# Kernel optimization log

Hardware: AMD Instinct MI355X
Metric: run time of the kernel (lower is better)

Reference implementation:

```python
import jax, jax.numpy as jnp
import numpy as np

HID = 256      # cfg.MODEL.YOSO.HIDDEN_DIM
NPROP = 100    # cfg.MODEL.YOSO.NUM_PROPOSALS
K1 = 3         # CONV_KERNEL_SIZE_1D
K2 = 1         # CONV_KERNEL_SIZE_2D
NCLS = 80      # NUM_CLASSES
NHEAD = 8

def layernorm(x, g, b, eps=1e-5):
    m = jnp.mean(x, -1, keepdims=True)
    v = jnp.var(x, -1, keepdims=True)
    return (x - m) * jax.lax.rsqrt(v + eps) * g + b

def dysep(query, value, Wl, bl, ng, nb):
    # dynamic depthwise conv (kernel K1 along feature axis, one kernel per proposal)
    # followed by dynamic pointwise NxN conv, per torch F.conv1d semantics (cross-correlation, 'same' pad)
    w = query @ Wl + bl                      # [B,N,N+K1]
    dw = w[..., :K1]                         # [B,N,K1] depthwise kernels
    pw = w[..., K1:]                         # [B,N,N]  pointwise mixing
    C = value.shape[-1]
    pad = K1 // 2
    vp = jnp.pad(value, ((0, 0), (0, 0), (pad, pad)))
    depth = sum(dw[..., k:k + 1] * vp[..., k:k + C] for k in range(K1))
    depth = jax.nn.relu(depth)
    point = jnp.einsum('bmn,bnc->bmc', pw, depth)
    return layernorm(point, ng, nb)

def mha(x, in_w, in_b, out_w, out_b):
    B, N, E = x.shape
    d = E // NHEAD
    qkv = x @ in_w + in_b
    q, k, v = jnp.split(qkv, 3, axis=-1)
    q = q.reshape(B, N, NHEAD, d)
    k = k.reshape(B, N, NHEAD, d)
    v = v.reshape(B, N, NHEAD, d)
    att = jnp.einsum('bqhd,bkhd->bhqk', q, k) / jnp.sqrt(jnp.asarray(d, x.dtype))
    att = jax.nn.softmax(att, axis=-1)
    o = jnp.einsum('bhqk,bkhd->bqhd', att, v).reshape(B, N, E)
    return o @ out_w + out_b

def setup_inputs() -> dict:
    key = jax.random.key(0)
    ks = iter(jax.random.split(key, 64))
    B, H, W = 8, 128, 128
    E = HID * K2 * K2
    nrm = lambda *s: jax.random.normal(next(ks), s, jnp.float32) * 0.02
    bias_value = -np.log((1 - 0.01) / 0.01)
    return dict(
        features=jax.random.normal(next(ks), (B, HID, H, W), jnp.float32),
        proposal_kernels=jax.random.normal(next(ks), (B, NPROP, E), jnp.float32),
        mask_preds=jax.random.normal(next(ks), (B, NPROP, H, W), jnp.float32),
        fW=nrm(E, NPROP + K1), fb=jnp.zeros(NPROP + K1), fng=jnp.ones(E), fnb=jnp.zeros(E),
        f_norm_g=jnp.ones(E), f_norm_b=jnp.zeros(E),
        kW=nrm(E, NPROP + K1), kb=jnp.zeros(NPROP + K1), kng=jnp.ones(E), knb=jnp.zeros(E),
        k_norm_g=jnp.ones(E), k_norm_b=jnp.zeros(E),
        attn_in_w=nrm(E, 3 * E), attn_in_b=jnp.zeros(3 * E),
        attn_out_w=nrm(E, E), attn_out_b=jnp.zeros(E),
        s_norm_g=jnp.ones(E), s_norm_b=jnp.zeros(E),
        ffn_w1=nrm(HID, 2048), ffn_b1=jnp.zeros(2048),
        ffn_w2=nrm(2048, HID), ffn_b2=jnp.zeros(HID),
        ffn_norm_g=jnp.ones(HID), ffn_norm_b=jnp.zeros(HID),
        cls_w=nrm(HID, HID), cls_ln_g=jnp.ones(HID), cls_ln_b=jnp.zeros(HID),
        fc_cls_w=nrm(HID, NCLS + 1), fc_cls_b=jnp.full((NCLS + 1,), bias_value, jnp.float32),
        mask_w=nrm(3, HID, HID), mask_ln_g=jnp.ones((3, HID)), mask_ln_b=jnp.zeros((3, HID)),
        fc_mask_w=nrm(HID, HID), fc_mask_b=jnp.zeros(HID),
        train_flag=1,
    )

def reference(features, proposal_kernels, mask_preds, fW, fb, fng, fnb, f_norm_g, f_norm_b,
              kW, kb, kng, knb, k_norm_g, k_norm_b,
              attn_in_w, attn_in_b, attn_out_w, attn_out_b, s_norm_g, s_norm_b,
              ffn_w1, ffn_b1, ffn_w2, ffn_b2, ffn_norm_g, ffn_norm_b,
              cls_w, cls_ln_g, cls_ln_b, fc_cls_w, fc_cls_b,
              mask_w, mask_ln_g, mask_ln_b, fc_mask_w, fc_mask_b, train_flag):
    B, C, H, W = features.shape
    hard = (jax.nn.sigmoid(mask_preds) > 0.5).astype(features.dtype)   # hard masks (no grad path)
    f = jnp.einsum('bnhw,bchw->bnc', hard, features)                   # mask-pooled features [B,N,E]
    k = proposal_kernels.reshape(B, NPROP, -1)
    f = layernorm(f + dysep(k, f, fW, fb, fng, fnb), f_norm_g, f_norm_b)
    kk = layernorm(f + dysep(k, f, kW, kb, kng, knb), k_norm_g, k_norm_b)
    kk = layernorm(kk + mha(kk, attn_in_w, attn_in_b, attn_out_w, attn_out_b), s_norm_g, s_norm_b)
    obj = jnp.transpose(kk.reshape(B, NPROP, HID, -1), (0, 1, 3, 2))   # [B,N,K2*K2,HID]
    h = jax.nn.relu(obj @ ffn_w1 + ffn_b1)
    obj = layernorm(obj + (h @ ffn_w2 + ffn_b2), ffn_norm_g, ffn_norm_b)
    cls_feat = obj.sum(-2)                                             # [B,N,HID]
    mask_feat = obj
    if train_flag:
        cls_feat = jax.nn.relu(layernorm(cls_feat @ cls_w, cls_ln_g, cls_ln_b))
        cls_score = (cls_feat @ fc_cls_w + fc_cls_b).reshape(B, NPROP, -1)
    else:
        cls_score = None
    for i in range(mask_w.shape[0]):
        mask_feat = jax.nn.relu(layernorm(mask_feat @ mask_w[i], mask_ln_g[i], mask_ln_b[i]))
    mask_kernels = (mask_feat @ fc_mask_w + fc_mask_b)[:, :, 0, :]     # squeeze(2), K2*K2==1
    new_mask_preds = jnp.einsum('bqc,bchw->bqhw', mask_kernels, features)
    obj_out = jnp.transpose(obj, (0, 1, 3, 2)).reshape(B, NPROP, HID, K2, K2)
    return (cls_score, new_mask_preds, obj_out)
```

## Files before the change

kernel.cpp:

```cpp
#include <hip/hip_runtime.h>

typedef float f32x4 __attribute__((ext_vector_type(4)));
typedef short bfrag __attribute__((ext_vector_type(8)));
typedef short sh4 __attribute__((ext_vector_type(4)));

__device__ __forceinline__ unsigned short f2bf(float x) {
  unsigned int u = __float_as_uint(x);
  return (unsigned short)((u + 0x7FFFu + ((u >> 16) & 1u)) >> 16);
}
__device__ __forceinline__ float bf2f(unsigned short u) {
  return __uint_as_float(((unsigned int)u) << 16);
}
__device__ __forceinline__ float wred_sum(float v) {
#pragma unroll
  for (int o = 32; o > 0; o >>= 1) v += __shfl_xor(v, o);
  return v;
}
__device__ __forceinline__ float wred_max(float v) {
#pragma unroll
  for (int o = 32; o > 0; o >>= 1) v = fmaxf(v, __shfl_xor(v, o));
  return v;
}

struct Prep12 {
  const float* s[12];
  int K[12];
  int N[12];
  int base[12];
  int doff[12];
};

__global__ __launch_bounds__(256) void prep_w(Prep12 p, unsigned short* wt) {
  int t = blockIdx.x;
  int wi = 0;
#pragma unroll
  for (int i = 0; i < 11; ++i)
    if (t >= p.base[i + 1]) wi = i + 1;
  int lt = t - p.base[wi];
  int K = p.K[wi], N = p.N[wi];
  int tkn = (K + 31) >> 5;
  int tk = lt % tkn, tn = lt / tkn;
  __shared__ float tile[32][33];
  const float* src = p.s[wi];
#pragma unroll
  for (int i = 0; i < 4; ++i) {
    int flat = i * 256 + threadIdx.x;
    int kl = flat >> 5, nl = flat & 31;
    int k = tk * 32 + kl, n = tn * 32 + nl;
    tile[kl][nl] = (k < K && n < N) ? src[(size_t)k * N + n] : 0.f;
  }
  __syncthreads();
  unsigned short* dst = wt + p.doff[wi];
#pragma unroll
  for (int i = 0; i < 4; ++i) {
    int flat = i * 256 + threadIdx.x;
    int nl = flat >> 5, kl = flat & 31;
    int k = tk * 32 + kl, n = tn * 32 + nl;
    if (k < K && n < N) {
      int np = (wi < 2) ? ((n >= 3) ? n - 3 : n + 100) : n;
      dst[(size_t)np * K + k] = f2bf(tile[kl][nl]);
    }
  }
}

__global__ __launch_bounds__(256) void prep_bias(const float* __restrict__ fb_,
                                                 const float* __restrict__ kb_,
                                                 float* __restrict__ bf,
                                                 float* __restrict__ bk) {
  int t = threadIdx.x;
  if (t < 103) {
    int np = (t >= 3) ? t - 3 : t + 100;
    bf[np] = fb_[t];
    bk[np] = kb_[t];
  }
  if (t == 103) { bf[103] = 0.f; bk[103] = 0.f; }
}

template <int ABF, int OBF>
__global__ __launch_bounds__(256) void gemm_mf(const void* Av,
                                               const unsigned short* __restrict__ Wt,
                                               const float* __restrict__ bias,
                                               void* Cv, int M, int K, int N, int ldc, int relu) {
  __shared__ short Al[64 * 72];
  __shared__ short Wl[64 * 72];
  int tid = threadIdx.x;
  int r0 = blockIdx.x * 64;
  int c0 = blockIdx.y * 64;
  int w = tid >> 6, lane = tid & 63, quad = lane >> 4, l15 = lane & 15;

  f32x4 acc[4];
#pragma unroll
  for (int mt = 0; mt < 4; ++mt) {
    acc[mt][0] = 0.f; acc[mt][1] = 0.f; acc[mt][2] = 0.f; acc[mt][3] = 0.f;
  }

  for (int k0 = 0; k0 < K; k0 += 64) {
    if (ABF) {
      const unsigned short* A = (const unsigned short*)Av;
#pragma unroll
      for (int p = 0; p < 2; ++p) {
        int flat = p * 256 + tid;
        int row = flat >> 3, k8 = flat & 7;
        bfrag v;
        if (r0 + row < M)
          v = *(const bfrag*)(A + (size_t)(r0 + row) * K + k0 + k8 * 8);
        else
          v = (bfrag)(short)0;
        *(bfrag*)(Al + row * 72 + k8 * 8) = v;
      }
    } else {
      const float* A = (const float*)Av;
#pragma unroll
      for (int p = 0; p < 4; ++p) {
        int flat = p * 256 + tid;
        int row = flat >> 4, c4 = flat & 15;
        sh4 o4;
        if (r0 + row < M) {
          float4 v = *(const float4*)(A + (size_t)(r0 + row) * K + k0 + c4 * 4);
          o4[0] = (short)f2bf(v.x); o4[1] = (short)f2bf(v.y);
          o4[2] = (short)f2bf(v.z); o4[3] = (short)f2bf(v.w);
        } else {
          o4[0] = 0; o4[1] = 0; o4[2] = 0; o4[3] = 0;
        }
        *(sh4*)(Al + row * 72 + c4 * 4) = o4;
      }
    }
#pragma unroll
    for (int p = 0; p < 2; ++p) {
      int flat = p * 256 + tid;
      int row = flat >> 3, k8 = flat & 7;
      bfrag v;
      if (c0 + row < N)
        v = *(const bfrag*)(Wt + (size_t)(c0 + row) * K + k0 + k8 * 8);
      else
        v = (bfrag)(short)0;
      *(bfrag*)(Wl + row * 72 + k8 * 8) = v;
    }
    __syncthreads();
#pragma unroll
    for (int kk = 0; kk < 2; ++kk) {
      bfrag bv = *(const bfrag*)(Wl + (w * 16 + l15) * 72 + kk * 32 + quad * 8);
#pragma unroll
      for (int mt = 0; mt < 4; ++mt) {
        bfrag av = *(const bfrag*)(Al + (mt * 16 + l15) * 72 + kk * 32 + quad * 8);
        acc[mt] = __builtin_amdgcn_mfma_f32_16x16x32_bf16(av, bv, acc[mt], 0, 0, 0);
      }
    }
    __syncthreads();
  }
  int col = c0 + w * 16 + l15;
  if (col < N) {
    float bv = bias ? bias[col] : 0.f;
#pragma unroll
    for (int mt = 0; mt < 4; ++mt)
#pragma unroll
      for (int r = 0; r < 4; ++r) {
        int m = r0 + mt * 16 + quad * 4 + r;
        if (m < M) {
          float v = acc[mt][r] + bv;
          if (relu) v = fmaxf(v, 0.f);
          if (OBF)
            ((unsigned short*)Cv)[(size_t)m * ldc + col] = f2bf(v);
          else
            ((float*)Cv)[(size_t)m * ldc + col] = v;
        }
      }
  }
}

__global__ __launch_bounds__(512, 4) void phaseA(const float* __restrict__ mask,
                                                 const float* __restrict__ feat,
                                                 float* __restrict__ partial) {
  int tid = threadIdx.x;
  int ks = blockIdx.x;
  int ct = blockIdx.y;
  int b  = blockIdx.z;
  __shared__ short Al[112 * 136];
  __shared__ short Bl[128 * 136];
  int w = tid >> 6, lane = tid & 63, quad = lane >> 4, l15 = lane & 15;

  f32x4 acc[7];
#pragma unroll
  for (int mt = 0; mt < 7; ++mt) {
    acc[mt][0] = 0.f; acc[mt][1] = 0.f; acc[mt][2] = 0.f; acc[mt][3] = 0.f;
  }

  int k0 = ks * 512;
  for (int st = 0; st < 4; ++st) {
    int kb = k0 + st * 128;
#pragma unroll
    for (int p = 0; p < 7; ++p) {
      int flat = p * 512 + tid;
      int row = flat >> 5, c4 = flat & 31;
      sh4 o4;
      if (row < 100) {
        float4 v = *(const float4*)(mask + (size_t)(b * 100 + row) * 16384 + kb + c4 * 4);
        o4[0] = (v.x > 0.f) ? (short)0x3F80 : (short)0;
        o4[1] = (v.y > 0.f) ? (short)0x3F80 : (short)0;
        o4[2] = (v.z > 0.f) ? (short)0x3F80 : (short)0;
        o4[3] = (v.w > 0.f) ? (short)0x3F80 : (short)0;
      } else {
        o4[0] = 0; o4[1] = 0; o4[2] = 0; o4[3] = 0;
      }
      *(sh4*)(Al + row * 136 + c4 * 4) = o4;
    }
#pragma unroll
    for (int p = 0; p < 8; ++p) {
      int flat = p * 512 + tid;
      int row = flat >> 5, c4 = flat & 31;
      float4 v = *(const float4*)(feat + (size_t)(b * 256 + ct * 128 + row) * 16384 + kb + c4 * 4);
      sh4 o4;
      o4[0] = (short)f2bf(v.x); o4[1] = (short)f2bf(v.y);
      o4[2] = (short)f2bf(v.z); o4[3] = (short)f2bf(v.w);
      *(sh4*)(Bl + row * 136 + c4 * 4) = o4;
    }
    __syncthreads();
#pragma unroll
    for (int kk = 0; kk < 4; ++kk) {
      bfrag bv = *(const bfrag*)(Bl + (w * 16 + l15) * 136 + kk * 32 + quad * 8);
#pragma unroll
      for (int mt = 0; mt < 7; ++mt) {
        bfrag av = *(const bfrag*)(Al + (mt * 16 + l15) * 136 + kk * 32 + quad * 8);
        acc[mt] = __builtin_amdgcn_mfma_f32_16x16x32_bf16(av, bv, acc[mt], 0, 0, 0);
      }
    }
    __syncthreads();
  }
  float* pb = partial + (size_t)(b * 32 + ks) * (100 * 256) + ct * 128 + w * 16 + l15;
#pragma unroll
  for (int mt = 0; mt < 7; ++mt)
#pragma unroll
    for (int r = 0; r < 4; ++r) {
      int m = mt * 16 + quad * 4 + r;
      if (m < 100) pb[(size_t)m * 256] = acc[mt][r];
    }
}

__global__ __launch_bounds__(256) void reduceA(const float* __restrict__ partial,
                                               float* __restrict__ fm) {
  int gid = blockIdx.x * 256 + threadIdx.x;
  int c = gid & 255, row = gid >> 8;
  int b = row / 100, n = row % 100;
  float s = 0.f;
#pragma unroll
  for (int ks = 0; ks < 32; ++ks)
    s += partial[((size_t)(b * 32 + ks) * 100 + n) * 256 + c];
  fm[(size_t)row * 256 + c] = s;
}

__global__ __launch_bounds__(256) void pointdw(const float* __restrict__ fm,
                                               const float* __restrict__ wbuf,
                                               float* __restrict__ point) {
  int tid = threadIdx.x;
  int b = blockIdx.y, c0 = blockIdx.x * 32;
  __shared__ float dl[100 * 33];
  for (int flat = tid; flat < 3200; flat += 256) {
    int n = flat >> 5, cl = flat & 31, c = c0 + cl;
    const float* fr = fm + (size_t)(b * 100 + n) * 256;
    const float* wr = wbuf + (size_t)(b * 100 + n) * 104;
    float x0 = (c > 0) ? fr[c - 1] : 0.f;
    float x1 = fr[c];
    float x2 = (c < 255) ? fr[c + 1] : 0.f;
    float d = wr[100] * x0 + wr[101] * x1 + wr[102] * x2;
    dl[n * 33 + cl] = fmaxf(d, 0.f);
  }
  __syncthreads();
  int cl = tid & 31, mg = tid >> 5;
  for (int m = mg; m < 100; m += 8) {
    const float4* pw4 = (const float4*)(wbuf + (size_t)(b * 100 + m) * 104);
    float a = 0.f;
#pragma unroll
    for (int n4 = 0; n4 < 25; ++n4) {
      float4 wv = pw4[n4];
      a += wv.x * dl[(n4 * 4 + 0) * 33 + cl] + wv.y * dl[(n4 * 4 + 1) * 33 + cl]
         + wv.z * dl[(n4 * 4 + 2) * 33 + cl] + wv.w * dl[(n4 * 4 + 3) * 33 + cl];
    }
    point[(size_t)(b * 100 + m) * 256 + c0 + cl] = a;
  }
}

__global__ __launch_bounds__(256) void ln2_kernel(const float* __restrict__ x,
                                                  const float* __restrict__ resid,
                                                  const float* __restrict__ g1, const float* __restrict__ b1,
                                                  const float* __restrict__ g2, const float* __restrict__ b2,
                                                  float* __restrict__ out) {
  int tid = threadIdx.x;
  int row = blockIdx.x * 4 + (tid >> 6);
  int lane = tid & 63;
  size_t base = (size_t)row * 256 + lane * 4;
  float4 v = *(const float4*)(x + base);
  float mean = wred_sum(v.x + v.y + v.z + v.w) * (1.f / 256.f);
  float d0 = v.x - mean, d1 = v.y - mean, d2 = v.z - mean, d3 = v.w - mean;
  float rs = rsqrtf(wred_sum(d0 * d0 + d1 * d1 + d2 * d2 + d3 * d3) * (1.f / 256.f) + 1e-5f);
  float4 gv = *(const float4*)(g1 + lane * 4);
  float4 bv = *(const float4*)(b1 + lane * 4);
  float4 rv = *(const float4*)(resid + base);
  float y0 = rv.x + d0 * rs * gv.x + bv.x;
  float y1 = rv.y + d1 * rs * gv.y + bv.y;
  float y2 = rv.z + d2 * rs * gv.z + bv.z;
  float y3 = rv.w + d3 * rs * gv.w + bv.w;
  float mean2 = wred_sum(y0 + y1 + y2 + y3) * (1.f / 256.f);
  float e0 = y0 - mean2, e1 = y1 - mean2, e2 = y2 - mean2, e3 = y3 - mean2;
  float rs2 = rsqrtf(wred_sum(e0 * e0 + e1 * e1 + e2 * e2 + e3 * e3) * (1.f / 256.f) + 1e-5f);
  float4 g2v = *(const float4*)(g2 + lane * 4);
  float4 b2v = *(const float4*)(b2 + lane * 4);
  float4 o;
  o.x = e0 * rs2 * g2v.x + b2v.x;
  o.y = e1 * rs2 * g2v.y + b2v.y;
  o.z = e2 * rs2 * g2v.z + b2v.z;
  o.w = e3 * rs2 * g2v.w + b2v.w;
  *(float4*)(out + base) = o;
}

__global__ __launch_bounds__(256) void ln_kernel(const float* __restrict__ x,
                                                 const float* __restrict__ res,
                                                 const float* __restrict__ g, const float* __restrict__ bb,
                                                 float* __restrict__ out, int relu,
                                                 float* __restrict__ copy2) {
  int tid = threadIdx.x;
  int row = blockIdx.x * 4 + (tid >> 6);
  int lane = tid & 63;
  size_t base = (size_t)row * 256 + lane * 4;
  float4 v = *(const float4*)(x + base);
  if (res) {
    float4 rv = *(const float4*)(res + base);
    v.x += rv.x; v.y += rv.y; v.z += rv.z; v.w += rv.w;
  }
  float mean = wred_sum(v.x + v.y + v.z + v.w) * (1.f / 256.f);
  float d0 = v.x - mean, d1 = v.y - mean, d2 = v.z - mean, d3 = v.w - mean;
  float rs = rsqrtf(wred_sum(d0 * d0 + d1 * d1 + d2 * d2 + d3 * d3) * (1.f / 256.f) + 1e-5f);
  float4 gv = *(const float4*)(g + lane * 4);
  float4 bv = *(const float4*)(bb + lane * 4);
  float4 o;
  o.x = d0 * rs * gv.x + bv.x;
  o.y = d1 * rs * gv.y + bv.y;
  o.z = d2 * rs * gv.z + bv.z;
  o.w = d3 * rs * gv.w + bv.w;
  if (relu) {
    o.x = fmaxf(o.x, 0.f); o.y = fmaxf(o.y, 0.f);
    o.z = fmaxf(o.z, 0.f); o.w = fmaxf(o.w, 0.f);
  }
  *(float4*)(out + base) = o;
  if (copy2) *(float4*)(copy2 + base) = o;
}

__global__ __launch_bounds__(256) void attn_kernel(const float* __restrict__ qkv,
                                                   float* __restrict__ obuf) {
  int tid = threadIdx.x;
  int b = blockIdx.y, h = blockIdx.x;
  __shared__ float ktj[100 * 32];
  __shared__ unsigned short vl[100 * 32];
  __shared__ float sl[100 * 100];
  const float* base = qkv + (size_t)b * 100 * 768;
  for (int flat = tid; flat < 3200; flat += 256) {
    int j = flat >> 5, dd = flat & 31;
    ktj[j * 32 + dd] = base[(size_t)j * 768 + 256 + h * 32 + dd];
    vl[j * 32 + dd] = f2bf(base[(size_t)j * 768 + 512 + h * 32 + dd]);
  }
  __syncthreads();
  {
    int i = tid >> 1;
    int jh = (tid & 1) * 50;
    int qi = (i < 100) ? i : 0;
    const float4* q4 = (const float4*)(base + (size_t)qi * 768 + h * 32);
    float4 q[8];
#pragma unroll
    for (int d4 = 0; d4 < 8; ++d4) q[d4] = q4[d4];
    if (i < 100) {
      for (int jj = 0; jj < 50; ++jj) {
        int j = jh + jj;
        const float4* kr = (const float4*)(ktj + j * 32);
        float a = 0.f;
#pragma unroll
        for (int d4 = 0; d4 < 8; ++d4) {
          float4 kv = kr[d4];
          a += q[d4].x * kv.x + q[d4].y * kv.y + q[d4].z * kv.z + q[d4].w * kv.w;
        }
        sl[i * 100 + j] = a * 0.17677669529663687f;
      }
    }
  }
  __syncthreads();
  int w = tid >> 6, lane = tid & 63;
  for (int r = w; r < 100; r += 4) {
    float x0 = sl[r * 100 + lane];
    float x1 = (lane + 64 < 100) ? sl[r * 100 + lane + 64] : -1e30f;
    float mx = wred_max(fmaxf(x0, x1));
    float e0 = __expf(x0 - mx);
    float e1 = (lane + 64 < 100) ? __expf(x1 - mx) : 0.f;
    float inv = 1.f / wred_sum(e0 + e1);
    sl[r * 100 + lane] = e0 * inv;
    if (lane + 64 < 100) sl[r * 100 + lane + 64] = e1 * inv;
  }
  __syncthreads();
  for (int flat = tid; flat < 3200; flat += 256) {
    int i = flat >> 5, dd = flat & 31;
    float a = 0.f;
#pragma unroll 4
    for (int j = 0; j < 100; ++j) a += sl[i * 100 + j] * bf2f(vl[j * 32 + dd]);
    obuf[(size_t)(b * 100 + i) * 256 + h * 32 + dd] = a;
  }
}

__global__ __launch_bounds__(256) void phaseE(const float* __restrict__ mk,
                                              const float* __restrict__ feat,
                                              float* __restrict__ out) {
  int tid = threadIdx.x;
  int b = blockIdx.y;
  int hw0 = blockIdx.x * 128;
  __shared__ short Al[112 * 264];
#pragma unroll
  for (int p = 0; p < 28; ++p) {
    int flat = p * 256 + tid;
    int row = flat >> 6, c4 = flat & 63;
    sh4 o4;
    if (row < 100) {
      float4 v = *(const float4*)(mk + (size_t)(b * 100 + row) * 256 + c4 * 4);
      o4[0] = (short)f2bf(v.x); o4[1] = (short)f2bf(v.y);
      o4[2] = (short)f2bf(v.z); o4[3] = (short)f2bf(v.w);
    } else {
      o4[0] = 0; o4[1] = 0; o4[2] = 0; o4[3] = 0;
    }
    *(sh4*)(Al + row * 264 + c4 * 4) = o4;
  }
  __syncthreads();
  int w = tid >> 6, lane = tid & 63, quad = lane >> 4, l15 = lane & 15;
  f32x4 acc[7][2];
#pragma unroll
  for (int mt = 0; mt < 7; ++mt)
#pragma unroll
    for (int nt = 0; nt < 2; ++nt) {
      acc[mt][nt][0] = 0.f; acc[mt][nt][1] = 0.f; acc[mt][nt][2] = 0.f; acc[mt][nt][3] = 0.f;
    }
  size_t fb = (size_t)b * 256 * 16384;
  int hwl = hw0 + w * 32 + l15;
  for (int kk = 0; kk < 8; ++kk) {
    bfrag bv[2];
#pragma unroll
    for (int nt = 0; nt < 2; ++nt) {
#pragma unroll
      for (int j = 0; j < 8; ++j) {
        float v = feat[fb + (size_t)(kk * 32 + quad * 8 + j) * 16384 + hwl + nt * 16];
        bv[nt][j] = (short)f2bf(v);
      }
    }
    bfrag av[7];
#pragma unroll
    for (int mt = 0; mt < 7; ++mt)
      av[mt] = *(const bfrag*)(Al + (mt * 16 + l15) * 264 + kk * 32 + quad * 8);
#pragma unroll
    for (int mt = 0; mt < 7; ++mt) {
      acc[mt][0] = __builtin_amdgcn_mfma_f32_16x16x32_bf16(av[mt], bv[0], acc[mt][0], 0, 0, 0);
      acc[mt][1] = __builtin_amdgcn_mfma_f32_16x16x32_bf16(av[mt], bv[1], acc[mt][1], 0, 0, 0);
    }
  }
#pragma unroll
  for (int mt = 0; mt < 7; ++mt)
#pragma unroll
    for (int nt = 0; nt < 2; ++nt)
#pragma unroll
      for (int r = 0; r < 4; ++r) {
        int m = mt * 16 + quad * 4 + r;
        if (m < 100)
          out[(size_t)(b * 100 + m) * 16384 + hw0 + w * 32 + nt * 16 + l15] = acc[mt][nt][r];
      }
}

extern "C" void kernel_launch(void* const* d_in, const int* in_sizes, int n_in,
                              void* d_out, int out_size, void* d_ws, size_t ws_size,
                              hipStream_t stream) {
  const float* feat    = (const float*)d_in[0];
  const float* prop    = (const float*)d_in[1];
  const float* maskp   = (const float*)d_in[2];
  const float* fW      = (const float*)d_in[3];
  const float* fb_     = (const float*)d_in[4];
  const float* fng     = (const float*)d_in[5];
  const float* fnb     = (const float*)d_in[6];
  const float* f_ng    = (const float*)d_in[7];
  const float* f_nb    = (const float*)d_in[8];
  const float* kW      = (const float*)d_in[9];
  const float* kb_     = (const float*)d_in[10];
  const float* kng     = (const float*)d_in[11];
  const float* knb     = (const float*)d_in[12];
  const float* k_ng    = (const float*)d_in[13];
  const float* k_nb    = (const float*)d_in[14];
  const float* aw_in   = (const float*)d_in[15];
  const float* ab_in   = (const float*)d_in[16];
  const float* aw_out  = (const float*)d_in[17];
  const float* ab_out  = (const float*)d_in[18];
  const float* s_ng    = (const float*)d_in[19];
  const float* s_nb    = (const float*)d_in[20];
  const float* w1      = (const float*)d_in[21];
  const float* b1      = (const float*)d_in[22];
  const float* w2      = (const float*)d_in[23];
  const float* b2      = (const float*)d_in[24];
  const float* ffn_ng  = (const float*)d_in[25];
  const float* ffn_nb  = (const float*)d_in[26];
  const float* cls_w   = (const float*)d_in[27];
  const float* cls_g   = (const float*)d_in[28];
  const float* cls_b   = (const float*)d_in[29];
  const float* fcclsw  = (const float*)d_in[30];
  const float* fcclsb  = (const float*)d_in[31];
  const float* mask_w  = (const float*)d_in[32];
  const float* mask_g  = (const float*)d_in[33];
  const float* mask_b  = (const float*)d_in[34];
  const float* fcmw    = (const float*)d_in[35];
  const float* fcmb    = (const float*)d_in[36];
  float* out = (float*)d_out;

  float* ws = (float*)d_ws;
  size_t off = 0;
  unsigned short* wt = (unsigned short*)(ws + off); off += 856192;
  float* fm     = ws + off; off += 204800;
  float* bias_f = ws + off; off += 104;
  float* bias_k = ws + off; off += 104;
  float* partial = ws + off;
  float* ub = partial;
  size_t uo = 0;
  float* wb   = ub + uo; uo += 83200;
  float* pt   = ub + uo; uo += 204800;
  float* fbuf = ub + uo; uo += 204800;
  float* kkb  = ub + uo; uo += 204800;
  float* qkvb = ub + uo; uo += 614400;
  float* ob   = ub + uo; uo += 204800;
  float* mo   = ub + uo; uo += 204800;
  float* kk2  = ub + uo; uo += 204800;
  float* t1   = ub + uo; uo += 204800;
  float* objb = ub + uo; uo += 204800;
  float* t2   = ub + uo; uo += 204800;
  float* mkb  = ub + uo; uo += 204800;
  unsigned short* ffn1b = (unsigned short*)(ub + uo); uo += 409600;

  const int wt_fW = 0, wt_kW = 26624, wt_ain = 53248, wt_aout = 249856;
  const int wt_w1 = 315392, wt_w2 = 839680, wt_cls = 1363968, wt_fccls = 1429504;
  const int wt_m0 = 1450240, wt_m1 = 1515776, wt_m2 = 1581312, wt_fcm = 1646848;

  float* out_cls  = out;
  float* out_mask = out + 64800;
  float* out_obj  = out + 64800 + 13107200;

  Prep12 p;
  const float* srcs[12] = {fW, kW, aw_in, aw_out, w1, w2, cls_w, fcclsw,
                           mask_w, mask_w + 65536, mask_w + 131072, fcmw};
  int Ks[12]    = {256, 256, 256, 256, 256, 2048, 256, 256, 256, 256, 256, 256};
  int Ns[12]    = {103, 103, 768, 256, 2048, 256, 256, 81, 256, 256, 256, 256};
  int doffs[12] = {wt_fW, wt_kW, wt_ain, wt_aout, wt_w1, wt_w2, wt_cls, wt_fccls,
                   wt_m0, wt_m1, wt_m2, wt_fcm};
  int tb = 0;
  for (int i = 0; i < 12; ++i) {
    p.s[i] = srcs[i]; p.K[i] = Ks[i]; p.N[i] = Ns[i]; p.doff[i] = doffs[i];
    p.base[i] = tb;
    tb += ((Ks[i] + 31) / 32) * ((Ns[i] + 31) / 32);
  }
  prep_w<<<tb, 256, 0, stream>>>(p, wt);
  prep_bias<<<1, 256, 0, stream>>>(fb_, kb_, bias_f, bias_k);

  phaseA<<<dim3(32, 2, 8), 512, 0, stream>>>(maskp, feat, partial);
  reduceA<<<800, 256, 0, stream>>>(partial, fm);
  gemm_mf<0, 0><<<dim3(13, 2), 256, 0, stream>>>(prop, wt + wt_fW, bias_f, wb, 800, 256, 103, 104, 0);
  pointdw<<<dim3(8, 8), 256, 0, stream>>>(fm, wb, pt);
  ln2_kernel<<<200, 256, 0, stream>>>(pt, fm, fng, fnb, f_ng, f_nb, fbuf);
  gemm_mf<0, 0><<<dim3(13, 2), 256, 0, stream>>>(prop, wt + wt_kW, bias_k, wb, 800, 256, 103, 104, 0);
  pointdw<<<dim3(8, 8), 256, 0, stream>>>(fbuf, wb, pt);
  ln2_kernel<<<200, 256, 0, stream>>>(pt, fbuf, kng, knb, k_ng, k_nb, kkb);
  gemm_mf<0, 0><<<dim3(13, 12), 256, 0, stream>>>(kkb, wt + wt_ain, ab_in, qkvb, 800, 256, 768, 768, 0);
  attn_kernel<<<dim3(8, 8), 256, 0, stream>>>(qkvb, ob);
  gemm_mf<0, 0><<<dim3(13, 4), 256, 0, stream>>>(ob, wt + wt_aout, ab_out, mo, 800, 256, 256, 256, 0);
  ln_kernel<<<200, 256, 0, stream>>>(mo, kkb, s_ng, s_nb, kk2, 0, nullptr);
  gemm_mf<0, 1><<<dim3(13, 32), 256, 0, stream>>>(kk2, wt + wt_w1, b1, ffn1b, 800, 256, 2048, 2048, 1);
  gemm_mf<1, 0><<<dim3(13, 4), 256, 0, stream>>>(ffn1b, wt + wt_w2, b2, t1, 800, 2048, 256, 256, 0);
  ln_kernel<<<200, 256, 0, stream>>>(t1, kk2, ffn_ng, ffn_nb, objb, 0, out_obj);
  gemm_mf<0, 0><<<dim3(13, 4), 256, 0, stream>>>(objb, wt + wt_cls, nullptr, t1, 800, 256, 256, 256, 0);
  ln_kernel<<<200, 256, 0, stream>>>(t1, nullptr, cls_g, cls_b, t2, 1, nullptr);
  gemm_mf<0, 0><<<dim3(13, 2), 256, 0, stream>>>(t2, wt + wt_fccls, fcclsb, out_cls, 800, 256, 81, 81, 0);
  gemm_mf<0, 0><<<dim3(13, 4), 256, 0, stream>>>(objb, wt + wt_m0, nullptr, t1, 800, 256, 256, 256, 0);
  ln_kernel<<<200, 256, 0, stream>>>(t1, nullptr, mask_g, mask_b, t2, 1, nullptr);
  gemm_mf<0, 0><<<dim3(13, 4), 256, 0, stream>>>(t2, wt + wt_m1, nullptr, t1, 800, 256, 256, 256, 0);
  ln_kernel<<<200, 256, 0, stream>>>(t1, nullptr, mask_g + 256, mask_b + 256, t2, 1, nullptr);
  gemm_mf<0, 0><<<dim3(13, 4), 256, 0, stream>>>(t2, wt + wt_m2, nullptr, t1, 800, 256, 256, 256, 0);
  ln_kernel<<<200, 256, 0, stream>>>(t1, nullptr, mask_g + 512, mask_b + 512, t2, 1, nullptr);
  gemm_mf<0, 0><<<dim3(13, 4), 256, 0, stream>>>(t2, wt + wt_fcm, fcmb, mkb, 800, 256, 256, 256, 0);
  phaseE<<<dim3(128, 8), 256, 0, stream>>>(mkb, feat, out_mask);
}
```

Measured before the change: 679.2 us.

## Double-buffer phaseA LDS tiles with register prefetch of next K-slice

```diff
diff --git a/kernel.cpp b/kernel.cpp
--- a/kernel.cpp
+++ b/kernel.cpp
@@ -175,9 +175,14 @@
   int ks = blockIdx.x;
   int ct = blockIdx.y;
   int b  = blockIdx.z;
-  __shared__ short Al[112 * 136];
-  __shared__ short Bl[128 * 136];
+  __shared__ short Al[2][112 * 72];
+  __shared__ short Bl[2][128 * 72];
   int w = tid >> 6, lane = tid & 63, quad = lane >> 4, l15 = lane & 15;
+
+  int rbase = tid >> 4;
+  int c4 = tid & 15;
+  const float* mrow = mask + (size_t)(b * 100 + rbase) * 16384 + c4 * 4;
+  const float* frow = feat + (size_t)(b * 256 + ct * 128 + rbase) * 16384 + c4 * 4;
 
   f32x4 acc[7];
 #pragma unroll
@@ -185,47 +190,89 @@
     acc[mt][0] = 0.f; acc[mt][1] = 0.f; acc[mt][2] = 0.f; acc[mt][3] = 0.f;
   }
 
+  for (int z = tid; z < 384; z += 512) {
+    int bufi = z / 192, rem = z % 192;
+    sh4 zz; zz[0] = 0; zz[1] = 0; zz[2] = 0; zz[3] = 0;
+    *(sh4*)(&Al[bufi][(100 + (rem >> 4)) * 72 + (rem & 15) * 4]) = zz;
+  }
+
   int k0 = ks * 512;
-  for (int st = 0; st < 4; ++st) {
-    int kb = k0 + st * 128;
-#pragma unroll
-    for (int p = 0; p < 7; ++p) {
-      int flat = p * 512 + tid;
-      int row = flat >> 5, c4 = flat & 31;
-      sh4 o4;
+  {
+    float4 apf[4], bpf[4];
+#pragma unroll
+    for (int p = 0; p < 4; ++p) {
+      int row = rbase + 32 * p;
+      if (row < 100) apf[p] = *(const float4*)(mrow + (size_t)p * 32 * 16384 + k0);
+      bpf[p] = *(const float4*)(frow + (size_t)p * 32 * 16384 + k0);
+    }
+#pragma unroll
+    for (int p = 0; p < 4; ++p) {
+      int row = rbase + 32 * p;
       if (row < 100) {
-        float4 v = *(const float4*)(mask + (size_t)(b * 100 + row) * 16384 + kb + c4 * 4);
-        o4[0] = (v.x > 0.f) ? (short)0x3F80 : (short)0;
-        o4[1] = (v.y > 0.f) ? (short)0x3F80 : (short)0;
-        o4[2] = (v.z > 0.f) ? (short)0x3F80 : (short)0;
-        o4[3] = (v.w > 0.f) ? (short)0x3F80 : (short)0;
-      } else {
-        o4[0] = 0; o4[1] = 0; o4[2] = 0; o4[3] = 0;
-      }
-      *(sh4*)(Al + row * 136 + c4 * 4) = o4;
-    }
-#pragma unroll
-    for (int p = 0; p < 8; ++p) {
-      int flat = p * 512 + tid;
-      int row = flat >> 5, c4 = flat & 31;
-      float4 v = *(const float4*)(feat + (size_t)(b * 256 + ct * 128 + row) * 16384 + kb + c4 * 4);
-      sh4 o4;
-      o4[0] = (short)f2bf(v.x); o4[1] = (short)f2bf(v.y);
-      o4[2] = (short)f2bf(v.z); o4[3] = (short)f2bf(v.w);
-      *(sh4*)(Bl + row * 136 + c4 * 4) = o4;
+        sh4 o4;
+        o4[0] = (apf[p].x > 0.f) ? (short)0x3F80 : (short)0;
+        o4[1] = (apf[p].y > 0.f) ? (short)0x3F80 : (short)0;
+        o4[2] = (apf[p].z > 0.f) ? (short)0x3F80 : (short)0;
+        o4[3] = (apf[p].w > 0.f) ? (short)0x3F80 : (short)0;
+        *(sh4*)(&Al[0][row * 72 + c4 * 4]) = o4;
+      }
+      sh4 o4b;
+      o4b[0] = (short)f2bf(bpf[p].x);
+      o4b[1] = (short)f2bf(bpf[p].y);
+      o4b[2] = (short)f2bf(bpf[p].z);
+      o4b[3] = (short)f2bf(bpf[p].w);
+      *(sh4*)(&Bl[0][row * 72 + c4 * 4]) = o4b;
+    }
+  }
+  __syncthreads();
+
+  int cur = 0;
+  for (int st = 0; st < 8; ++st) {
+    float4 apf[4], bpf[4];
+    if (st < 7) {
+      int kb = k0 + (st + 1) * 64;
+#pragma unroll
+      for (int p = 0; p < 4; ++p) {
+        int row = rbase + 32 * p;
+        if (row < 100) apf[p] = *(const float4*)(mrow + (size_t)p * 32 * 16384 + kb);
+        bpf[p] = *(const float4*)(frow + (size_t)p * 32 * 16384 + kb);
+      }
+    }
+#pragma unroll
+    for (int kk = 0; kk < 2; ++kk) {
+      bfrag bv = *(const bfrag*)(&Bl[cur][(w * 16 + l15) * 72 + kk * 32 + quad * 8]);
+#pragma unroll
+      for (int mt = 0; mt < 7; ++mt) {
+        bfrag av = *(const bfrag*)(&Al[cur][(mt * 16 + l15) * 72 + kk * 32 + quad * 8]);
+        acc[mt] = __builtin_amdgcn_mfma_f32_16x16x32_bf16(av, bv, acc[mt], 0, 0, 0);
+      }
+    }
+    __builtin_amdgcn_sched_barrier(0);
+    if (st < 7) {
+      int nxt = cur ^ 1;
+#pragma unroll
+      for (int p = 0; p < 4; ++p) {
+        int row = rbase + 32 * p;
+        if (row < 100) {
+          sh4 o4;
+          o4[0] = (apf[p].x > 0.f) ? (short)0x3F80 : (short)0;
+          o4[1] = (apf[p].y > 0.f) ? (short)0x3F80 : (short)0;
+          o4[2] = (apf[p].z > 0.f) ? (short)0x3F80 : (short)0;
+          o4[3] = (apf[p].w > 0.f) ? (short)0x3F80 : (short)0;
+          *(sh4*)(&Al[nxt][row * 72 + c4 * 4]) = o4;
+        }
+        sh4 o4b;
+        o4b[0] = (short)f2bf(bpf[p].x);
+        o4b[1] = (short)f2bf(bpf[p].y);
+        o4b[2] = (short)f2bf(bpf[p].z);
+        o4b[3] = (short)f2bf(bpf[p].w);
+        *(sh4*)(&Bl[nxt][row * 72 + c4 * 4]) = o4b;
+      }
     }
     __syncthreads();
-#pragma unroll
-    for (int kk = 0; kk < 4; ++kk) {
-      bfrag bv = *(const bfrag*)(Bl + (w * 16 + l15) * 136 + kk * 32 + quad * 8);
-#pragma unroll
-      for (int mt = 0; mt < 7; ++mt) {
-        bfrag av = *(const bfrag*)(Al + (mt * 16 + l15) * 136 + kk * 32 + quad * 8);
-        acc[mt] = __builtin_amdgcn_mfma_f32_16x16x32_bf16(av, bv, acc[mt], 0, 0, 0);
-      }
-    }
-    __syncthreads();
-  }
+    cur ^= 1;
+  }
+
   float* pb = partial + (size_t)(b * 32 + ks) * (100 * 256) + ct * 128 + w * 16 + l15;
 #pragma unroll
   for (int mt = 0; mt < 7; ++mt)
```

Result: no change. 680.5 us (+0.2%).
